# Kernel optimization log

Hardware: AMD Instinct MI355X
Metric: run time of the kernel (lower is better)

The kernel has to match this reference:

```python
import jax, jax.numpy as jnp
import numpy as np

NUM_T = 1000
B, N = 16, 2048
M = 8192


def _cosine_alphas_cumprod(T=NUM_T, s=0.008):
    # Faithful to ColdDiffusion.cosine_beta_schedule + cumprod of (1 - betas)
    x = np.linspace(0.0, T, T + 1)
    ac = np.cos((x / T + s) / (1 + s) * np.pi * 0.5) ** 2
    ac = ac / ac[0]
    betas = np.clip(1.0 - ac[1:] / ac[:-1], 0.0001, 0.9999)
    return np.cumprod(1.0 - betas)


def setup_inputs() -> dict:
    key = jax.random.key(0)
    k1, k2, k3 = jax.random.split(key, 3)
    x_start = jax.random.normal(k1, (B, N, 4, 2), dtype=jnp.float32)
    anchors = jax.random.normal(k2, (M, 4, 2), dtype=jnp.float32)
    t = jax.random.randint(k3, (B,), 0, NUM_T)
    ac = _cosine_alphas_cumprod()
    sqrt_alphas_cumprod = jnp.asarray(np.sqrt(ac), dtype=jnp.float32)
    sqrt_one_minus_alphas_cumprod = jnp.asarray(np.sqrt(1.0 - ac), dtype=jnp.float32)
    return {
        "x_start": x_start,
        "anchors": anchors,
        "sqrt_alphas_cumprod": sqrt_alphas_cumprod,
        "sqrt_one_minus_alphas_cumprod": sqrt_one_minus_alphas_cumprod,
        "t": t,
    }


def reference(x_start, anchors, sqrt_alphas_cumprod, sqrt_one_minus_alphas_cumprod, t):
    # q_sample with anchor matching, fully batched (no Python loop over B).
    Bq, Nq = x_start.shape[:2]
    xf = x_start.reshape(Bq, Nq, -1)            # [B,N,8]
    af = anchors.reshape(anchors.shape[0], -1)  # [M,8]
    scores = jnp.einsum('bnd,md->bnm', xf, af) * (-2.0) + jnp.sum(af * af, axis=-1)  # [B,N,M]
    idx = jnp.argmin(scores, axis=-1)           # [B,N]
    matched = anchors[idx]                      # [B,N,4,2] gather
    sa = sqrt_alphas_cumprod[t][:, None, None, None]                 # [B,1,1,1]
    sb = sqrt_one_minus_alphas_cumprod[t][:, None, None, None]       # [B,1,1,1]
    return sa * x_start + sb * matched
```

## Files before the change

### kernel.cpp

```cpp
#include <hip/hip_runtime.h>
#include <stdint.h>

#define B_      16
#define N_      2048
#define M_      8192
#define ROWS    (B_ * N_)
#define D_      8

#define QUARTERS 8
#define APQ     (M_ / QUARTERS)
#define CHUNK   256
#define NCHUNK  (APQ / CHUNK)
#define TPC     (CHUNK / 16)
#define WROWS   64
#define BROWS_A 256
#define GRIDX   (ROWS / BROWS_A)

#define OFF_NH  0
#define OFF_NM  4096
#define OFF_NL  8192
#define OFF_HN  12288
#define CHUNK_BYTES 13312
#define SMEM_BYTES 36864


typedef short bf16x8 __attribute__((ext_vector_type(8)));
typedef float f32x4  __attribute__((ext_vector_type(4)));

__device__ __forceinline__ unsigned short f2bf(float f) {
    unsigned u = __float_as_uint(f);
    u += 0x7FFFu + ((u >> 16) & 1u);
    return (unsigned short)(u >> 16);
}
__device__ __forceinline__ float bf2f(unsigned short h) {
    return __uint_as_float(((unsigned)h) << 16);
}

__global__ __launch_bounds__(256) void prep_kernel(
    const float* __restrict__ anchors, char* __restrict__ pk)
{
    const int a = blockIdx.x * 256 + threadIdx.x;
    const float4* pa = (const float4*)(anchors + (size_t)a * D_);
    const float4 g0 = pa[0], g1 = pa[1];
    float nv[8] = {-g0.x, -g0.y, -g0.z, -g0.w, -g1.x, -g1.y, -g1.z, -g1.w};
    bf16x8 vh, vm, vl;
    #pragma unroll
    for (int k = 0; k < 8; ++k) {
        unsigned short h = f2bf(nv[k]);
        float r1 = nv[k] - bf2f(h);
        unsigned short m = f2bf(r1);
        float r2 = r1 - bf2f(m);
        unsigned short l = f2bf(r2);
        vh[k] = (short)h; vm[k] = (short)m; vl[k] = (short)l;
    }
    char* base = pk + (size_t)(a >> 8) * CHUNK_BYTES;
    const int i = a & 255;
    *(bf16x8*)(base + OFF_NH + i * 16) = vh;
    *(bf16x8*)(base + OFF_NM + i * 16) = vm;
    *(bf16x8*)(base + OFF_NL + i * 16) = vl;
    float nr = nv[0] * nv[0];
    #pragma unroll
    for (int k = 1; k < 8; ++k) nr = fmaf(nv[k], nv[k], nr);
    *(float*)(base + OFF_HN + i * 4) = 0.5f * nr;
}

__global__ __launch_bounds__(256)
__attribute__((amdgpu_waves_per_eu(4, 4)))
void argmin_mfma_kernel(
    const float* __restrict__ x,
    const char*  __restrict__ pk,
    float* __restrict__ wsv)
{
    __shared__ __align__(16) char smem[SMEM_BYTES];

    const int tid  = threadIdx.x;
    const int wave = tid >> 6;
    const int lane = tid & 63;
    const int n    = lane & 15;
    const int kb   = lane >> 4;

    const int quarter = blockIdx.y;
    const int wrow0   = blockIdx.x * BROWS_A + wave * WROWS;

    const char* srcq = pk + (size_t)quarter * NCHUNK * CHUNK_BYTES;

    {
        char* bufw = smem;
        #pragma unroll
        for (int sg = 0; sg < 3; ++sg) {
            const int seg = (wave + sg * 4) * 1024;
            __builtin_amdgcn_global_load_lds(srcq + seg + lane * 16,
                                             bufw + seg, 16, 0, 0);
        }
        if (wave == 0)
            __builtin_amdgcn_global_load_lds(srcq + 12288 + lane * 16,
                                             bufw + 12288, 16, 0, 0);
    }

    bf16x8 A1[4], A2[4];
    #pragma unroll
    for (int rt = 0; rt < 4; ++rt) {
        const int row = wrow0 + rt * 16 + n;
        const float4* px = (const float4*)(x + (size_t)row * D_);
        const float4 lo = px[0], hi = px[1];
        const float v[8] = {lo.x, lo.y, lo.z, lo.w, hi.x, hi.y, hi.z, hi.w};
        const bool odd = (kb & 1);
        const bool is2 = (kb == 2);
        #pragma unroll
        for (int k = 0; k < 8; ++k) {
            unsigned short xh = f2bf(v[k]);
            float r1 = v[k] - bf2f(xh);
            unsigned short xm = f2bf(r1);
            float r2 = r1 - bf2f(xm);
            unsigned short xl = f2bf(r2);
            A1[rt][k] = (short)(odd ? xm : xh);
            A2[rt][k] = (short)(odd ? xl : (is2 ? xm : xh));
        }
    }

    const int o1 = ((kb < 2) ? OFF_NH : OFF_NM) + n * 16;
    const int o2 = ((kb == 1) ? OFF_NH : (kb == 3) ? OFF_NM : OFF_NL) + n * 16;
    const int oh = OFF_HN + n * 4;

    float best[4][4];
    #pragma unroll
    for (int rt = 0; rt < 4; ++rt)
        #pragma unroll
        for (int q = 0; q < 4; ++q) best[rt][q] = 3.4e38f;

    __syncthreads();

    #pragma unroll 1
    for (int c = 0; c < NCHUNK; ++c) {
        const char* bufr = smem + (c & 1) * CHUNK_BYTES;

        if (c < NCHUNK - 1) {
            char* bufw = smem + ((c & 1) ^ 1) * CHUNK_BYTES;
            const char* g = srcq + (size_t)(c + 1) * CHUNK_BYTES;
            #pragma unroll
            for (int sg = 0; sg < 3; ++sg) {
                const int seg = (wave + sg * 4) * 1024;
                __builtin_amdgcn_global_load_lds(g + seg + lane * 16,
                                                 bufw + seg, 16, 0, 0);
            }
            if (wave == 0)
                __builtin_amdgcn_global_load_lds(g + 12288 + lane * 16,
                                                 bufw + 12288, 16, 0, 0);
        }

        #pragma unroll 2
        for (int tt = 0; tt < TPC; ++tt) {
            const bf16x8 b1 = *(const bf16x8*)(bufr + o1 + tt * 256);
            const bf16x8 b2 = *(const bf16x8*)(bufr + o2 + tt * 256);
            const float  hn = *(const float*)(bufr + oh + tt * 64);
            const f32x4 cvec = {hn, hn, hn, hn};
            #pragma unroll
            for (int rt = 0; rt < 4; ++rt) {
                f32x4 acc = __builtin_amdgcn_mfma_f32_16x16x32_bf16(A1[rt], b1, cvec, 0, 0, 0);
                acc = __builtin_amdgcn_mfma_f32_16x16x32_bf16(A2[rt], b2, acc, 0, 0, 0);
                #pragma unroll
                for (int q = 0; q < 4; ++q)
                    best[rt][q] = fminf(best[rt][q], acc[q]);
            }
        }

        __syncthreads();
    }

    #pragma unroll
    for (int rt = 0; rt < 4; ++rt) {
        #pragma unroll
        for (int q = 0; q < 4; ++q) {
            float bv = best[rt][q];
            #pragma unroll
            for (int m = 1; m < 16; m <<= 1)
                bv = fminf(bv, __shfl_xor(bv, m));
            if ((lane & 15) == 0) {
                const int row = wrow0 + rt * 16 + (lane >> 4) * 4 + q;
                wsv[(size_t)quarter * ROWS + row] = bv;
            }
        }
    }
}

#define BQ 256
__global__ __launch_bounds__(256) void rescan_kernel(
    const float* __restrict__ x,
    const float* __restrict__ anchors,
    const float* __restrict__ sa_tab,
    const float* __restrict__ sb_tab,
    const int*   __restrict__ t,
    const float* __restrict__ wsv,
    float* __restrict__ out)
{
    __shared__ __align__(16) float sAq[APQ * D_];
    __shared__ unsigned short rowlist[BQ];
    __shared__ int cnt;

    const int tid  = threadIdx.x;
    const int q    = blockIdx.y;
    const int row0 = blockIdx.x * BQ;

    if (tid == 0) cnt = 0;
    __syncthreads();

    {
        const int row = row0 + tid;
        float bv = wsv[row];
        int   bq = 0;
        #pragma unroll
        for (int qq = 1; qq < QUARTERS; ++qq) {
            const float v = wsv[(size_t)qq * ROWS + row];
            const bool c = v < bv;
            bv = c ? v : bv;
            bq = c ? qq : bq;
        }
        if (bq == q) {
            const int p = atomicAdd(&cnt, 1);
            rowlist[p] = (unsigned short)tid;
        }
    }
    __syncthreads();
    const int nrows = cnt;
    if (nrows == 0) return;

    {
        const float4* gA = (const float4*)(anchors + (size_t)q * APQ * D_);
        float4* b = (float4*)sAq;
        #pragma unroll
        for (int i = 0; i < 8; ++i)
            b[tid + i * 256] = gA[tid + i * 256];
    }
    __syncthreads();

    const int g   = tid & 7;
    const int grp = tid >> 3;
    for (int i = grp; i < nrows; i += 32) {
        const int row = row0 + rowlist[i];
        const float4* px = (const float4*)(x + (size_t)row * D_);
        const float4 xlo = px[0], xhi = px[1];
        const float X0 = xlo.x, X1 = xlo.y, X2 = xlo.z, X3 = xlo.w;
        const float X4 = xhi.x, X5 = xhi.y, X6 = xhi.z, X7 = xhi.w;

        float bs = 3.4e38f;
        int   bl = 0x7FFFFFFF;
        #pragma unroll 4
        for (int j = 0; j < APQ / 8; ++j) {
            const int al = j * 8 + g;
            const float4* pa = (const float4*)(&sAq[al * D_]);
            const float4 g0 = pa[0], g1 = pa[1];
            const float na0 = -g0.x, na1 = -g0.y, na2 = -g0.z, na3 = -g0.w;
            const float na4 = -g1.x, na5 = -g1.y, na6 = -g1.z, na7 = -g1.w;
            float nr = na0 * na0;
            nr = fmaf(na1, na1, nr);
            nr = fmaf(na2, na2, nr);
            nr = fmaf(na3, na3, nr);
            nr = fmaf(na4, na4, nr);
            nr = fmaf(na5, na5, nr);
            nr = fmaf(na6, na6, nr);
            nr = fmaf(na7, na7, nr);
            const float hn = 0.5f * nr;
            float s = fmaf(X0, na0, hn);
            s = fmaf(X1, na1, s);
            s = fmaf(X2, na2, s);
            s = fmaf(X3, na3, s);
            s = fmaf(X4, na4, s);
            s = fmaf(X5, na5, s);
            s = fmaf(X6, na6, s);
            s = fmaf(X7, na7, s);
            const bool lt = s < bs;
            bs = lt ? s  : bs;
            bl = lt ? al : bl;
        }
        #pragma unroll
        for (int m = 1; m < 8; m <<= 1) {
            const float ov = __shfl_xor(bs, m);
            const int   ol = __shfl_xor(bl, m);
            const bool take = (ov < bs) || (ov == bs && ol < bl);
            bs = take ? ov : bs;
            bl = take ? ol : bl;
        }

        if (g == 0) {
            const int bi = q * APQ + bl;
            const int b  = row >> 11;
            const int tb = t[b];
            const float sa = sa_tab[tb];
            const float sb = sb_tab[tb];
            const float4* pa = (const float4*)(&sAq[bl * D_]);
            const float4 a0 = pa[0], a1 = pa[1];
            (void)bi;
            float4 o0, o1;
            o0.x = fmaf(sa, xlo.x, sb * a0.x);
            o0.y = fmaf(sa, xlo.y, sb * a0.y);
            o0.z = fmaf(sa, xlo.z, sb * a0.z);
            o0.w = fmaf(sa, xlo.w, sb * a0.w);
            o1.x = fmaf(sa, xhi.x, sb * a1.x);
            o1.y = fmaf(sa, xhi.y, sb * a1.y);
            o1.z = fmaf(sa, xhi.z, sb * a1.z);
            o1.w = fmaf(sa, xhi.w, sb * a1.w);
            float4* po = (float4*)(out + (size_t)row * D_);
            po[0] = o0;
            po[1] = o1;
        }
    }
}

extern "C" void kernel_launch(void* const* d_in, const int* in_sizes, int n_in,
                              void* d_out, int out_size, void* d_ws, size_t ws_size,
                              hipStream_t stream) {
    const float* x       = (const float*)d_in[0];
    const float* anchors = (const float*)d_in[1];
    const float* sa_tab  = (const float*)d_in[2];
    const float* sb_tab  = (const float*)d_in[3];
    const int*   t       = (const int*)d_in[4];
    float* out = (float*)d_out;

    float* wsv = (float*)d_ws;
    char*  pk  = (char*)d_ws + (size_t)1024 * 1024;

    prep_kernel<<<M_ / 256, 256, 0, stream>>>(anchors, pk);

    dim3 gridA(GRIDX, QUARTERS);
    argmin_mfma_kernel<<<gridA, 256, 0, stream>>>(x, pk, wsv);

    dim3 gridB(ROWS / BQ, QUARTERS);
    rescan_kernel<<<gridB, 256, 0, stream>>>(
        x, anchors, sa_tab, sb_tab, t, wsv, out);
}
```

Measured before the change: 116.0 us.

## Record per-chunk minima so the exact rescan covers one 256-anchor chunk

The bf16 MFMA pass now writes a minimum score for every 256-anchor chunk rather than one per 1024-anchor group. The fp32 rescan picks the winning chunk per row from 32 candidates and rescans only those 256 anchors from global memory, instead of staging 1024 anchors in LDS per group. The rescan grid also drops its row-list compaction. The cost is a larger workspace (32 values per row, written once per chunk by the MFMA kernel) and a somewhat higher chance that bf16 rounding selects the wrong chunk.

```diff
diff --git a/kernel.cpp b/kernel.cpp
--- a/kernel.cpp
+++ b/kernel.cpp
@@ -11,6 +11,7 @@
 #define APQ     (M_ / QUARTERS)
 #define CHUNK   256
 #define NCHUNK  (APQ / CHUNK)
+#define NSPLIT  (M_ / CHUNK)
 #define TPC     (CHUNK / 16)
 #define WROWS   64
 #define BROWS_A 256
@@ -22,6 +23,9 @@
 #define OFF_HN  12288
 #define CHUNK_BYTES 13312
 #define SMEM_BYTES 36864
+
+#define TPR     8
+#define BROWS   32
 
 
 typedef short bf16x8 __attribute__((ext_vector_type(8)));
@@ -164,26 +168,26 @@
             }
         }
 
+        #pragma unroll
+        for (int rt = 0; rt < 4; ++rt) {
+            #pragma unroll
+            for (int q = 0; q < 4; ++q) {
+                float bv = best[rt][q];
+                #pragma unroll
+                for (int m = 1; m < 16; m <<= 1)
+                    bv = fminf(bv, __shfl_xor(bv, m));
+                if ((lane & 15) == 0) {
+                    const int row = wrow0 + rt * 16 + (lane >> 4) * 4 + q;
+                    wsv[(size_t)(quarter * NCHUNK + c) * ROWS + row] = bv;
+                }
+                best[rt][q] = 3.4e38f;
+            }
+        }
+
         __syncthreads();
     }
-
-    #pragma unroll
-    for (int rt = 0; rt < 4; ++rt) {
-        #pragma unroll
-        for (int q = 0; q < 4; ++q) {
-            float bv = best[rt][q];
-            #pragma unroll
-            for (int m = 1; m < 16; m <<= 1)
-                bv = fminf(bv, __shfl_xor(bv, m));
-            if ((lane & 15) == 0) {
-                const int row = wrow0 + rt * 16 + (lane >> 4) * 4 + q;
-                wsv[(size_t)quarter * ROWS + row] = bv;
-            }
-        }
-    }
-}
-
-#define BQ 256
+}
+
 __global__ __launch_bounds__(256) void rescan_kernel(
     const float* __restrict__ x,
     const float* __restrict__ anchors,
@@ -193,116 +197,97 @@
     const float* __restrict__ wsv,
     float* __restrict__ out)
 {
-    __shared__ __align__(16) float sAq[APQ * D_];
-    __shared__ unsigned short rowlist[BQ];
-    __shared__ int cnt;
-
     const int tid  = threadIdx.x;
-    const int q    = blockIdx.y;
-    const int row0 = blockIdx.x * BQ;
-
-    if (tid == 0) cnt = 0;
-    __syncthreads();
-
-    {
-        const int row = row0 + tid;
-        float bv = wsv[row];
-        int   bq = 0;
-        #pragma unroll
-        for (int qq = 1; qq < QUARTERS; ++qq) {
-            const float v = wsv[(size_t)qq * ROWS + row];
-            const bool c = v < bv;
-            bv = c ? v : bv;
-            bq = c ? qq : bq;
-        }
-        if (bq == q) {
-            const int p = atomicAdd(&cnt, 1);
-            rowlist[p] = (unsigned short)tid;
-        }
-    }
-    __syncthreads();
-    const int nrows = cnt;
-    if (nrows == 0) return;
-
-    {
-        const float4* gA = (const float4*)(anchors + (size_t)q * APQ * D_);
-        float4* b = (float4*)sAq;
-        #pragma unroll
-        for (int i = 0; i < 8; ++i)
-            b[tid + i * 256] = gA[tid + i * 256];
-    }
-    __syncthreads();
-
-    const int g   = tid & 7;
-    const int grp = tid >> 3;
-    for (int i = grp; i < nrows; i += 32) {
-        const int row = row0 + rowlist[i];
-        const float4* px = (const float4*)(x + (size_t)row * D_);
-        const float4 xlo = px[0], xhi = px[1];
-        const float X0 = xlo.x, X1 = xlo.y, X2 = xlo.z, X3 = xlo.w;
-        const float X4 = xhi.x, X5 = xhi.y, X6 = xhi.z, X7 = xhi.w;
-
-        float bs = 3.4e38f;
-        int   bl = 0x7FFFFFFF;
-        #pragma unroll 4
-        for (int j = 0; j < APQ / 8; ++j) {
-            const int al = j * 8 + g;
-            const float4* pa = (const float4*)(&sAq[al * D_]);
-            const float4 g0 = pa[0], g1 = pa[1];
-            const float na0 = -g0.x, na1 = -g0.y, na2 = -g0.z, na3 = -g0.w;
-            const float na4 = -g1.x, na5 = -g1.y, na6 = -g1.z, na7 = -g1.w;
-            float nr = na0 * na0;
-            nr = fmaf(na1, na1, nr);
-            nr = fmaf(na2, na2, nr);
-            nr = fmaf(na3, na3, nr);
-            nr = fmaf(na4, na4, nr);
-            nr = fmaf(na5, na5, nr);
-            nr = fmaf(na6, na6, nr);
-            nr = fmaf(na7, na7, nr);
-            const float hn = 0.5f * nr;
-            float s = fmaf(X0, na0, hn);
-            s = fmaf(X1, na1, s);
-            s = fmaf(X2, na2, s);
-            s = fmaf(X3, na3, s);
-            s = fmaf(X4, na4, s);
-            s = fmaf(X5, na5, s);
-            s = fmaf(X6, na6, s);
-            s = fmaf(X7, na7, s);
-            const bool lt = s < bs;
-            bs = lt ? s  : bs;
-            bl = lt ? al : bl;
-        }
-        #pragma unroll
-        for (int m = 1; m < 8; m <<= 1) {
-            const float ov = __shfl_xor(bs, m);
-            const int   ol = __shfl_xor(bl, m);
-            const bool take = (ov < bs) || (ov == bs && ol < bl);
-            bs = take ? ov : bs;
-            bl = take ? ol : bl;
-        }
-
-        if (g == 0) {
-            const int bi = q * APQ + bl;
-            const int b  = row >> 11;
-            const int tb = t[b];
-            const float sa = sa_tab[tb];
-            const float sb = sb_tab[tb];
-            const float4* pa = (const float4*)(&sAq[bl * D_]);
-            const float4 a0 = pa[0], a1 = pa[1];
-            (void)bi;
-            float4 o0, o1;
-            o0.x = fmaf(sa, xlo.x, sb * a0.x);
-            o0.y = fmaf(sa, xlo.y, sb * a0.y);
-            o0.z = fmaf(sa, xlo.z, sb * a0.z);
-            o0.w = fmaf(sa, xlo.w, sb * a0.w);
-            o1.x = fmaf(sa, xhi.x, sb * a1.x);
-            o1.y = fmaf(sa, xhi.y, sb * a1.y);
-            o1.z = fmaf(sa, xhi.z, sb * a1.z);
-            o1.w = fmaf(sa, xhi.w, sb * a1.w);
-            float4* po = (float4*)(out + (size_t)row * D_);
-            po[0] = o0;
-            po[1] = o1;
-        }
+    const int g    = tid & (TPR - 1);
+    const int rloc = tid >> 3;
+    const int row  = blockIdx.x * BROWS + rloc;
+
+    float bs = 3.4e38f;
+    int   bsp = 0;
+    #pragma unroll
+    for (int k = 0; k < NSPLIT / TPR; ++k) {
+        const int s = g + k * TPR;
+        const float v = wsv[(size_t)s * ROWS + row];
+        const bool c = v < bs;
+        bs  = c ? v : bs;
+        bsp = c ? s : bsp;
+    }
+    #pragma unroll
+    for (int m = 1; m < TPR; m <<= 1) {
+        const float ov  = __shfl_xor(bs, m);
+        const int   osp = __shfl_xor(bsp, m);
+        const bool take = (ov < bs) || (ov == bs && osp < bsp);
+        bs  = take ? ov  : bs;
+        bsp = take ? osp : bsp;
+    }
+    const int base = bsp * CHUNK;
+
+    const float4* px = (const float4*)(x + (size_t)row * D_);
+    const float4 xlo = px[0], xhi = px[1];
+    const float X0 = xlo.x, X1 = xlo.y, X2 = xlo.z, X3 = xlo.w;
+    const float X4 = xhi.x, X5 = xhi.y, X6 = xhi.z, X7 = xhi.w;
+
+    float bv = 3.4e38f;
+    int   bi = 0x7FFFFFFF;
+    #pragma unroll 4
+    for (int j = 0; j < CHUNK / TPR; ++j) {
+        const int ai = base + j * TPR + g;
+        const float4* pa = (const float4*)(anchors + (size_t)ai * D_);
+        const float4 g0 = pa[0], g1 = pa[1];
+        const float na0 = -g0.x, na1 = -g0.y, na2 = -g0.z, na3 = -g0.w;
+        const float na4 = -g1.x, na5 = -g1.y, na6 = -g1.z, na7 = -g1.w;
+        float nr = na0 * na0;
+        nr = fmaf(na1, na1, nr);
+        nr = fmaf(na2, na2, nr);
+        nr = fmaf(na3, na3, nr);
+        nr = fmaf(na4, na4, nr);
+        nr = fmaf(na5, na5, nr);
+        nr = fmaf(na6, na6, nr);
+        nr = fmaf(na7, na7, nr);
+        const float hn = 0.5f * nr;
+        float s = fmaf(X0, na0, hn);
+        s = fmaf(X1, na1, s);
+        s = fmaf(X2, na2, s);
+        s = fmaf(X3, na3, s);
+        s = fmaf(X4, na4, s);
+        s = fmaf(X5, na5, s);
+        s = fmaf(X6, na6, s);
+        s = fmaf(X7, na7, s);
+        const bool lt = s < bv;
+        bv = lt ? s  : bv;
+        bi = lt ? ai : bi;
+    }
+    #pragma unroll
+    for (int m = 1; m < TPR; m <<= 1) {
+        const float ov = __shfl_xor(bv, m);
+        const int   oi = __shfl_xor(bi, m);
+        const bool take = (ov < bv) || (ov == bv && oi < bi);
+        bv = take ? ov : bv;
+        bi = take ? oi : bi;
+    }
+
+    if (g == 0) {
+        const int b  = row >> 11;
+        const int tb = t[b];
+        const float sa = sa_tab[tb];
+        const float sb = sb_tab[tb];
+
+        const float4* pa = (const float4*)(anchors + (size_t)bi * D_);
+        const float4 a0 = pa[0], a1 = pa[1];
+
+        float4 o0, o1;
+        o0.x = fmaf(sa, xlo.x, sb * a0.x);
+        o0.y = fmaf(sa, xlo.y, sb * a0.y);
+        o0.z = fmaf(sa, xlo.z, sb * a0.z);
+        o0.w = fmaf(sa, xlo.w, sb * a0.w);
+        o1.x = fmaf(sa, xhi.x, sb * a1.x);
+        o1.y = fmaf(sa, xhi.y, sb * a1.y);
+        o1.z = fmaf(sa, xhi.z, sb * a1.z);
+        o1.w = fmaf(sa, xhi.w, sb * a1.w);
+
+        float4* po = (float4*)(out + (size_t)row * D_);
+        po[0] = o0;
+        po[1] = o1;
     }
 }
 
@@ -317,14 +302,13 @@
     float* out = (float*)d_out;
 
     float* wsv = (float*)d_ws;
-    char*  pk  = (char*)d_ws + (size_t)1024 * 1024;
+    char*  pk  = (char*)d_ws + (size_t)4 * 1024 * 1024;
 
     prep_kernel<<<M_ / 256, 256, 0, stream>>>(anchors, pk);
 
     dim3 gridA(GRIDX, QUARTERS);
     argmin_mfma_kernel<<<gridA, 256, 0, stream>>>(x, pk, wsv);
 
-    dim3 gridB(ROWS / BQ, QUARTERS);
-    rescan_kernel<<<gridB, 256, 0, stream>>>(
+    rescan_kernel<<<ROWS / BROWS, 256, 0, stream>>>(
         x, anchors, sa_tab, sb_tab, t, wsv, out);
 }
```

After: 109.2 us. -5.9%, faster.
